# Kernel optimization log

Measured on AMD Instinct MI355X. Metric: run time of the kernel, lower is better.

## Reference

```python
import jax, jax.numpy as jnp
import numpy as np
from jax import lax

B, T, E, H, D, L = 2048, 512, 128, 8, 16, 3


def _ln(x, g, b):
    m = jnp.mean(x, -1, keepdims=True)
    v = jnp.var(x, -1, keepdims=True)
    return (x - m) / jnp.sqrt(v + 1e-5) * g + b


def _bn(x, g, b):  # eval-mode BatchNorm2d with running_mean=0, running_var=1
    return x * (g / np.sqrt(1.0 + 1e-5))[None, :, None, None] + b[None, :, None, None]


def _conv(x, w, b):  # 3x3 conv, padding=1, NCHW / OIHW
    y = lax.conv_general_dilated(x, w, (1, 1), 'SAME', dimension_numbers=('NCHW', 'OIHW', 'NCHW'))
    return y + b[None, :, None, None]


def _forward(enc_out, x1, x2, x3, c11_w, c11_b, bn11_g, bn11_b, c12_w, c12_b, bn12_g, bn12_b,
             fc1_w, fc1_b, c21_w, c21_b, bn21_g, bn21_b, fc2_w, fc2_b, fc_w, fc_b,
             wk, wq, wv, proj_w, proj_b, ln1_g, ln1_b, ln2_g, ln2_b, ln3_g, ln3_b, ln4_g, ln4_b,
             ff_w1, ff_b1, ff_w2, ff_b2, lnf_g, lnf_b, head_w, head_b):
    # StateNet -> query vector q: [B, E]
    h1 = jax.nn.relu(_bn(_conv(x1, c11_w, c11_b), bn11_g, bn11_b))
    h1 = jax.nn.relu(_bn(_conv(h1, c12_w, c12_b), bn12_g, bn12_b))
    h1 = jax.nn.relu(h1.reshape(h1.shape[0], -1) @ fc1_w + fc1_b)  # [B, 64]
    h2 = jax.nn.relu(_bn(_conv(x2, c21_w, c21_b), bn21_g, bn21_b))
    h2 = jax.nn.relu(h2.reshape(h2.shape[0], -1) @ fc2_w + fc2_b)  # [B, 16]
    q = jax.nn.relu(jnp.concatenate([h1, h2, x3], axis=-1) @ fc_w + fc_b)  # [B, E]

    for l in range(L):  # 3 structurally identical DecoderBlocks
        kx = _ln(enc_out, ln1_g[l], ln1_b[l])
        vx = _ln(enc_out, ln2_g[l], ln2_b[l])
        qx = _ln(q, ln3_g[l], ln3_b[l])
        K = (kx @ wk[l]).reshape(B, T, H, D)
        V = (vx @ wv[l]).reshape(B, T, H, D)
        Q = (qx @ wq[l]).reshape(B, H, D)
        # NOTE: original multiplies (not divides) by head_size**0.5 -- kept faithful.
        wei = jax.nn.softmax(jnp.einsum('bhd,bthd->bht', Q, K) * (D ** 0.5), axis=-1)
        att = jnp.einsum('bht,bthd->bhd', wei, V).reshape(B, E)
        q = q + att @ proj_w[l] + proj_b[l]
        h = _ln(q, ln4_g[l], ln4_b[l])
        q = q + jax.nn.gelu(h @ ff_w1[l] + ff_b1[l], approximate=False) @ ff_w2[l] + ff_b2[l]

    x = _ln(q, lnf_g, lnf_b)
    return x @ head_w + head_b  # discard head logits [B, 37]


def setup_inputs():
    key = jax.random.key(0)
    ks = iter(jax.random.split(key, 32))
    r = lambda *s: jax.random.normal(next(ks), s, jnp.float32) * 0.02
    z = lambda *s: jnp.zeros(s, jnp.float32)
    o = lambda *s: jnp.ones(s, jnp.float32)
    return dict(
        enc_out=jax.random.normal(next(ks), (B, T, E), jnp.float32),
        x1=jax.random.normal(next(ks), (B, 3, 37, 1), jnp.float32),
        x2=jax.random.normal(next(ks), (B, 7, 4, 1), jnp.float32),
        x3=jax.random.normal(next(ks), (B, 4), jnp.float32),
        c11_w=r(8, 3, 3, 3), c11_b=z(8), bn11_g=o(8), bn11_b=z(8),
        c12_w=r(8, 8, 3, 3), c12_b=z(8), bn12_g=o(8), bn12_b=z(8),
        fc1_w=r(296, 64), fc1_b=z(64),
        c21_w=r(8, 7, 3, 3), c21_b=z(8), bn21_g=o(8), bn21_b=z(8),
        fc2_w=r(32, 16), fc2_b=z(16),
        fc_w=r(84, E), fc_b=z(E),
        wk=r(L, E, E), wq=r(L, E, E), wv=r(L, E, E),
        proj_w=r(L, E, E), proj_b=z(L, E),
        ln1_g=o(L, E), ln1_b=z(L, E), ln2_g=o(L, E), ln2_b=z(L, E),
        ln3_g=o(L, E), ln3_b=z(L, E), ln4_g=o(L, E), ln4_b=z(L, E),
        ff_w1=r(L, E, 4 * E), ff_b1=z(L, 4 * E), ff_w2=r(L, 4 * E, E), ff_b2=z(L, E),
        lnf_g=o(E), lnf_b=z(E),
        head_w=r(E, 37), head_b=z(37),
    )


def reference(enc_out, x1, x2, x3, c11_w, c11_b, bn11_g, bn11_b, c12_w, c12_b, bn12_g, bn12_b,
              fc1_w, fc1_b, c21_w, c21_b, bn21_g, bn21_b, fc2_w, fc2_b, fc_w, fc_b,
              wk, wq, wv, proj_w, proj_b, ln1_g, ln1_b, ln2_g, ln2_b, ln3_g, ln3_b, ln4_g, ln4_b,
              ff_w1, ff_b1, ff_w2, ff_b2, lnf_g, lnf_b, head_w, head_b):
    return _forward(enc_out, x1, x2, x3, c11_w, c11_b, bn11_g, bn11_b, c12_w, c12_b, bn12_g, bn12_b,
                    fc1_w, fc1_b, c21_w, c21_b, bn21_g, bn21_b, fc2_w, fc2_b, fc_w, fc_b,
                    wk, wq, wv, proj_w, proj_b, ln1_g, ln1_b, ln2_g, ln2_b, ln3_g, ln3_b, ln4_g, ln4_b,
                    ff_w1, ff_b1, ff_w2, ff_b2, lnf_g, lnf_b, head_w, head_b)
```

## Files before the change

kernel.cpp:

```cpp
#include <hip/hip_runtime.h>
#include <math.h>

typedef unsigned int u32;
typedef unsigned short u16;
typedef unsigned char u8;
typedef __attribute__((ext_vector_type(4))) float f32x4;
typedef __attribute__((ext_vector_type(8))) short bf16x8;

__device__ __forceinline__ u16 f2b(float f){ u32 u=__float_as_uint(f); u=(u+0x7fffu+((u>>16)&1u))>>16; return (u16)u; }
__device__ __forceinline__ float b2f(u16 h){ return __uint_as_float(((u32)h)<<16); }

struct P {
  const float* in[43];
  float* out;
  float* q;
  u16*   S;
  const u16* xr;
  u16*   xw;
  int    xstrideu;
};

__global__ __launch_bounds__(512) void k_state(P p){
  __shared__ float sx1[112];
  __shared__ float sx2[32];
  __shared__ float sa[296];
  __shared__ float sb[296];
  __shared__ float sc2[32];
  __shared__ float sh1[64];
  __shared__ float sh2[16];
  __shared__ float red[512];
  int tid=threadIdx.x; int b=blockIdx.x;
  const float rs_bn = rsqrtf(1.0f+1e-5f);
  const float* x1 = p.in[1] + (size_t)b*111;
  const float* x2 = p.in[2] + (size_t)b*28;
  if (tid<111) sx1[tid]=x1[tid];
  if (tid>=128 && tid<156) sx2[tid-128]=x2[tid-128];
  __syncthreads();
  if (tid<296){
    int cc=tid/37, i=tid-cc*37;
    const float* wgt=p.in[4];
    float acc=p.in[5][cc];
    #pragma unroll
    for(int ic=0;ic<3;++ic)
      #pragma unroll
      for(int kh=0;kh<3;++kh){
        int ii=i+kh-1;
        if((unsigned)ii<37u) acc+=wgt[((cc*3+ic)*3+kh)*3+1]*sx1[ic*37+ii];
      }
    acc=acc*(p.in[6][cc]*rs_bn)+p.in[7][cc];
    sa[tid]=fmaxf(acc,0.f);
  }
  if (tid>=296 && tid<328){
    int o=tid-296, cc=o>>2, i=o&3;
    const float* wgt=p.in[14];
    float acc=p.in[15][cc];
    for(int ic=0;ic<7;++ic)
      for(int kh=0;kh<3;++kh){
        int ii=i+kh-1;
        if((unsigned)ii<4u) acc+=wgt[((cc*7+ic)*3+kh)*3+1]*sx2[ic*4+ii];
      }
    acc=acc*(p.in[16][cc]*rs_bn)+p.in[17][cc];
    sc2[o]=fmaxf(acc,0.f);
  }
  __syncthreads();
  if (tid<296){
    int cc=tid/37, i=tid-cc*37;
    const float* wgt=p.in[8];
    float acc=p.in[9][cc];
    #pragma unroll
    for(int ic=0;ic<8;++ic)
      #pragma unroll
      for(int kh=0;kh<3;++kh){
        int ii=i+kh-1;
        if((unsigned)ii<37u) acc+=wgt[((cc*8+ic)*3+kh)*3+1]*sa[ic*37+ii];
      }
    acc=acc*(p.in[10][cc]*rs_bn)+p.in[11][cc];
    sb[tid]=fmaxf(acc,0.f);
  }
  if (tid>=480 && tid<496){
    int o=tid-480;
    const float* wgt=p.in[18];
    float acc=p.in[19][o];
    for(int k=0;k<32;++k) acc+=sc2[k]*wgt[k*16+o];
    sh2[o]=fmaxf(acc,0.f);
  }
  __syncthreads();
  {
    int o=tid>>3, j=tid&7;
    const float* wgt=p.in[12];
    float part=0.f;
    for(int m=0;m<37;++m){ int k=j*37+m; part+=sb[k]*wgt[k*64+o]; }
    red[o*8+j]=part;
  }
  __syncthreads();
  if (tid<64){
    float acc=p.in[13][tid];
    #pragma unroll
    for(int j=0;j<8;++j) acc+=red[tid*8+j];
    sh1[tid]=fmaxf(acc,0.f);
  }
  __syncthreads();
  if (tid<128){
    const float* wgt=p.in[20];
    const float* x3=p.in[3]+(size_t)b*4;
    float acc=p.in[21][tid];
    for(int k=0;k<64;++k) acc+=sh1[k]*wgt[k*128+tid];
    for(int k=0;k<16;++k) acc+=sh2[k]*wgt[(64+k)*128+tid];
    #pragma unroll
    for(int k=0;k<4;++k) acc+=x3[k]*wgt[(80+k)*128+tid];
    p.q[(size_t)b*128+tid]=fmaxf(acc,0.f);
  }
}

__global__ __launch_bounds__(256) void k_xhat(P p){
  int b = blockIdx.x; int tid=threadIdx.x; int w=tid>>6, lane=tid&63;
  int r2 = lane>>5, c = lane&31;
  const float* enc = p.in[0] + (size_t)b*512*128;
  u16* xw = p.xw + (size_t)b*512*p.xstrideu;
  for (int it=0; it<64; ++it){
    int row = w*128 + it*2 + r2;
    float4 v = *(const float4*)(enc + (size_t)row*128 + c*4);
    float s = v.x+v.y+v.z+v.w;
    float s2 = v.x*v.x+v.y*v.y+v.z*v.z+v.w*v.w;
    #pragma unroll
    for (int m=1; m<=16; m<<=1){ s+=__shfl_xor(s,m); s2+=__shfl_xor(s2,m); }
    float mean = s*(1.f/128.f);
    float rstd = rsqrtf(s2*(1.f/128.f)-mean*mean+1e-5f);
    u32 a = (u32)f2b((v.x-mean)*rstd) | ((u32)f2b((v.y-mean)*rstd)<<16);
    u32 bq= (u32)f2b((v.z-mean)*rstd) | ((u32)f2b((v.w-mean)*rstd)<<16);
    *(uint2*)(xw + (size_t)row*p.xstrideu + c*4) = make_uint2(a,bq);
  }
}

#define XS 136
__global__ __launch_bounds__(256,3) void k_attn(P p, int l){
  __shared__ u16 XH[128*XS];
  __shared__ u16 WT[16*XS];
  __shared__ u16 QK[16*XS];
  __shared__ float qxs[128], Qs[128], red[256];
  __shared__ float wred[64], sred[64], alphaL[16], mL[16], m_run[16], invL[16], st[2];
  int tid=threadIdx.x, w=tid>>6, lane=tid&63, l15=lane&15, q4=lane>>4;
  int b = blockIdx.x;
  const float* wk = p.in[22] + l*16384;
  const float* wq = p.in[23] + l*16384;
  const float* g1 = p.in[27] + l*128;
  const float* g2 = p.in[29] + l*128;
  const float* g3 = p.in[31] + l*128;
  const float* b3 = p.in[32] + l*128;
  const float* qg = p.q + (size_t)b*128;

  if (w==0){
    float x0=qg[lane], x1=qg[lane+64];
    float s=x0+x1, s2=x0*x0+x1*x1;
    #pragma unroll
    for(int m=1;m<=32;m<<=1){ s+=__shfl_xor(s,m); s2+=__shfl_xor(s2,m); }
    if(lane==0){ float mean=s*(1.f/128.f); st[0]=mean; st[1]=rsqrtf(s2*(1.f/128.f)-mean*mean+1e-5f); }
  }
  if (tid<16) m_run[tid] = -INFINITY;
  __syncthreads();
  if (tid<128) qxs[tid] = (qg[tid]-st[0])*st[1]*g3[tid] + b3[tid];
  __syncthreads();
  {
    int o = tid & 127, kh = tid>>7;
    float acc=0;
    const float* wp = wq + kh*64*128 + o;
    #pragma unroll 8
    for (int e=0;e<64;++e) acc += qxs[kh*64+e]*wp[e*128];
    red[tid]=acc;
  }
  __syncthreads();
  if (tid<128) Qs[tid]=red[tid]+red[tid+128];
  for (int i=tid; i<8*XS; i+=256) QK[8*XS+i]=0;
  __syncthreads();
  {
    int h = tid>>5, e0=(tid&31)*4;
    float Qh[16];
    #pragma unroll
    for(int d=0;d<16;++d) Qh[d]=Qs[h*16+d];
    #pragma unroll
    for(int j=0;j<4;++j){
      int e=e0+j;
      const float* wr = wk + e*128 + h*16;
      float4 w0=*(const float4*)(wr), w1=*(const float4*)(wr+4), w2=*(const float4*)(wr+8), w3=*(const float4*)(wr+12);
      float acc = Qh[0]*w0.x+Qh[1]*w0.y+Qh[2]*w0.z+Qh[3]*w0.w
                + Qh[4]*w1.x+Qh[5]*w1.y+Qh[6]*w1.z+Qh[7]*w1.w
                + Qh[8]*w2.x+Qh[9]*w2.y+Qh[10]*w2.z+Qh[11]*w2.w
                + Qh[12]*w3.x+Qh[13]*w3.y+Qh[14]*w3.z+Qh[15]*w3.w;
      QK[h*XS+e] = f2b(acc*g1[e]*4.f);
    }
  }
  __syncthreads();
  bf16x8 qkf[4];
  #pragma unroll
  for(int ks=0;ks<4;++ks) qkf[ks]=*(const bf16x8*)(QK + l15*XS + ks*32 + q4*8);

  const u16* xrow = p.xr + (size_t)b*512*p.xstrideu;
  f32x4 wa0={0,0,0,0}, wa1={0,0,0,0};
  float s_part=0.f;
  for (int ch=0; ch<4; ++ch){
    __syncthreads();
    {
      const u16* src = xrow + (size_t)ch*128*p.xstrideu;
      #pragma unroll
      for(int i=0;i<8;++i){
        int idx = tid + i*256;
        int row = idx>>4, oct = idx&15;
        uint4 v = *(const uint4*)(src + (size_t)row*p.xstrideu + oct*8);
        *(uint4*)(XH + row*XS + oct*8) = v;
      }
    }
    __syncthreads();
    f32x4 c0={0,0,0,0}, c1={0,0,0,0};
    #pragma unroll
    for(int ks=0;ks<4;++ks){
      bf16x8 a0 = *(const bf16x8*)(XH + (w*32+l15)*XS + ks*32 + q4*8);
      bf16x8 a1 = *(const bf16x8*)(XH + (w*32+16+l15)*XS + ks*32 + q4*8);
      c0 = __builtin_amdgcn_mfma_f32_16x16x32_bf16(a0, qkf[ks], c0, 0,0,0);
      c1 = __builtin_amdgcn_mfma_f32_16x16x32_bf16(a1, qkf[ks], c1, 0,0,0);
    }
    float mx = fmaxf(fmaxf(fmaxf(c0[0],c0[1]),fmaxf(c0[2],c0[3])),
                     fmaxf(fmaxf(c1[0],c1[1]),fmaxf(c1[2],c1[3])));
    mx = fmaxf(mx, __shfl_xor(mx,16)); mx = fmaxf(mx, __shfl_xor(mx,32));
    if (lane<16) wred[w*16+lane]=mx;
    __syncthreads();
    if (tid<16){
      float m_new = fmaxf(fmaxf(wred[tid],wred[16+tid]),fmaxf(wred[32+tid],wred[48+tid]));
      m_new = fmaxf(m_new, m_run[tid]);
      alphaL[tid] = __expf(m_run[tid]-m_new);
      mL[tid]=m_new; m_run[tid]=m_new;
    }
    __syncthreads();
    float mnew = mL[l15];
    float e0v[4], e1v[4];
    float ssum=0.f;
    #pragma unroll
    for(int r=0;r<4;++r){ e0v[r]=__expf(c0[r]-mnew); e1v[r]=__expf(c1[r]-mnew); ssum+=e0v[r]+e1v[r]; }
    #pragma unroll
    for(int r=0;r<4;++r){
      WT[l15*XS + w*32 + q4*4 + r]      = f2b(e0v[r]);
      WT[l15*XS + w*32 + 16 + q4*4 + r] = f2b(e1v[r]);
    }
    ssum += __shfl_xor(ssum,16); ssum += __shfl_xor(ssum,32);
    s_part = s_part*alphaL[l15] + ssum;
    float ar0=alphaL[q4*4+0], ar1=alphaL[q4*4+1], ar2=alphaL[q4*4+2], ar3=alphaL[q4*4+3];
    wa0[0]*=ar0; wa0[1]*=ar1; wa0[2]*=ar2; wa0[3]*=ar3;
    wa1[0]*=ar0; wa1[1]*=ar1; wa1[2]*=ar2; wa1[3]*=ar3;
    __syncthreads();
    int eb0 = w*32 + l15, eb1 = w*32 + 16 + l15;
    #pragma unroll
    for(int ks=0;ks<4;++ks){
      bf16x8 aw = *(const bf16x8*)(WT + l15*XS + ks*32 + q4*8);
      bf16x8 bb0, bb1;
      #pragma unroll
      for(int j=0;j<8;++j){
        int t = ks*32 + q4*8 + j;
        bb0[j] = (short)XH[t*XS + eb0];
        bb1[j] = (short)XH[t*XS + eb1];
      }
      wa0 = __builtin_amdgcn_mfma_f32_16x16x32_bf16(aw, bb0, wa0, 0,0,0);
      wa1 = __builtin_amdgcn_mfma_f32_16x16x32_bf16(aw, bb1, wa1, 0,0,0);
    }
  }
  if (lane<16) sred[w*16+lane]=s_part;
  __syncthreads();
  if (tid<16) invL[tid] = 1.f/(sred[tid]+sred[16+tid]+sred[32+tid]+sred[48+tid]);
  __syncthreads();
  {
    int e0 = w*32 + l15, e1 = w*32+16+l15;
    float g20 = g2[e0], g21 = g2[e1];
    u16* Sb = p.S + (size_t)b*1024;
    #pragma unroll
    for(int r=0;r<4;++r){
      int h = q4*4+r;
      if (h<8){
        Sb[h*128 + e0] = f2b(wa0[r]*invL[h]*g20);
        Sb[h*128 + e1] = f2b(wa1[r]*invL[h]*g21);
      }
    }
  }
}

__global__ __launch_bounds__(256) void k_post(P p, int l){
  __shared__ u16 Ss[8*8*136];
  __shared__ float atts[8*128];
  __shared__ float qps[8*128];
  __shared__ float qx4[8*128];
  __shared__ float us[8*512];
  __shared__ float b2s[128];
  int tid=threadIdx.x; int r=tid>>5, c=tid&31;
  int b8 = blockIdx.x*8;
  const float* wv = p.in[24] + l*16384;
  const float* pw = p.in[25] + l*16384;
  const float* pb = p.in[26] + l*128;
  const float* b2 = p.in[30] + l*128;
  const float* g4 = p.in[33] + l*128;
  const float* b4 = p.in[34] + l*128;
  const float* f1 = p.in[35] + l*65536;
  const float* fb1= p.in[36] + l*512;
  const float* f2 = p.in[37] + l*65536;
  const float* fb2= p.in[38] + l*128;

  {
    const u16* Sg = p.S + (size_t)(b8+r)*1024;
    #pragma unroll
    for(int j=0;j<4;++j){
      int idx = c*8 + j*256;
      uint4 v = *(const uint4*)(Sg + idx);
      int h = idx>>7, e = idx&127;
      *(uint4*)(Ss + (r*8+h)*136 + e) = v;
    }
  }
  if (tid<128) b2s[tid]=b2[tid];
  __syncthreads();
  {
    int o0=c*4; int h=c>>2;
    float a0=0,a1=0,a2=0,a3=0, cc0=0,cc1=0,cc2=0,cc3=0;
    const u16* Sr = Ss + (r*8+h)*136;
    for(int e=0;e<128;++e){
      float sv=b2f(Sr[e]);
      float bv=b2s[e];
      float4 w4=*(const float4*)(wv + e*128 + o0);
      a0+=sv*w4.x; a1+=sv*w4.y; a2+=sv*w4.z; a3+=sv*w4.w;
      cc0+=bv*w4.x; cc1+=bv*w4.y; cc2+=bv*w4.z; cc3+=bv*w4.w;
    }
    atts[r*128+o0]=a0+cc0; atts[r*128+o0+1]=a1+cc1; atts[r*128+o0+2]=a2+cc2; atts[r*128+o0+3]=a3+cc3;
  }
  __syncthreads();
  {
    int o0=c*4;
    float a0=0,a1=0,a2=0,a3=0;
    for(int e=0;e<128;++e){
      float av=atts[r*128+e];
      float4 w4=*(const float4*)(pw + e*128 + o0);
      a0+=av*w4.x; a1+=av*w4.y; a2+=av*w4.z; a3+=av*w4.w;
    }
    float4 qv4=*(const float4*)(p.q + (size_t)(b8+r)*128 + o0);
    float4 pb4=*(const float4*)(pb + o0);
    qps[r*128+o0]  =qv4.x+a0+pb4.x;
    qps[r*128+o0+1]=qv4.y+a1+pb4.y;
    qps[r*128+o0+2]=qv4.z+a2+pb4.z;
    qps[r*128+o0+3]=qv4.w+a3+pb4.w;
  }
  __syncthreads();
  {
    float v0=qps[r*128+c], v1=qps[r*128+c+32], v2=qps[r*128+c+64], v3=qps[r*128+c+96];
    float s=v0+v1+v2+v3, s2=v0*v0+v1*v1+v2*v2+v3*v3;
    #pragma unroll
    for(int m=1;m<=16;m<<=1){ s+=__shfl_xor(s,m); s2+=__shfl_xor(s2,m); }
    float mean=s*(1.f/128.f), rstd=rsqrtf(s2*(1.f/128.f)-mean*mean+1e-5f);
    qx4[r*128+c]    =(v0-mean)*rstd*g4[c]+b4[c];
    qx4[r*128+c+32] =(v1-mean)*rstd*g4[c+32]+b4[c+32];
    qx4[r*128+c+64] =(v2-mean)*rstd*g4[c+64]+b4[c+64];
    qx4[r*128+c+96] =(v3-mean)*rstd*g4[c+96]+b4[c+96];
  }
  __syncthreads();
  {
    float acc[4][4]={};
    for(int e=0;e<128;++e){
      float xv=qx4[r*128+e];
      #pragma unroll
      for(int j=0;j<4;++j){
        float4 w4=*(const float4*)(f1 + e*512 + j*128 + c*4);
        acc[j][0]+=xv*w4.x; acc[j][1]+=xv*w4.y; acc[j][2]+=xv*w4.z; acc[j][3]+=xv*w4.w;
      }
    }
    #pragma unroll
    for(int j=0;j<4;++j)
      #pragma unroll
      for(int k=0;k<4;++k){
        int o=j*128+c*4+k;
        float u=acc[j][k]+fb1[o];
        us[r*512+o]=0.5f*u*(1.f+erff(u*0.70710678118654752f));
      }
  }
  __syncthreads();
  {
    int o0=c*4;
    float a0=0,a1=0,a2=0,a3=0;
    for(int e=0;e<512;++e){
      float uv=us[r*512+e];
      float4 w4=*(const float4*)(f2 + e*128 + o0);
      a0+=uv*w4.x; a1+=uv*w4.y; a2+=uv*w4.z; a3+=uv*w4.w;
    }
    float4 fb=*(const float4*)(fb2+o0);
    float* qp = p.q + (size_t)(b8+r)*128 + o0;
    float o0v=qps[r*128+o0]+a0+fb.x;
    float o1v=qps[r*128+o0+1]+a1+fb.y;
    float o2v=qps[r*128+o0+2]+a2+fb.z;
    float o3v=qps[r*128+o0+3]+a3+fb.w;
    float4 res; res.x=o0v; res.y=o1v; res.z=o2v; res.w=o3v;
    *(float4*)qp = res;
  }
}

__global__ __launch_bounds__(256) void k_head(P p){
  __shared__ float qx[8*128];
  int tid=threadIdx.x; int r=tid>>5, c=tid&31;
  int b8=blockIdx.x*8;
  const float* lg=p.in[39]; const float* lb=p.in[40];
  const float* hw=p.in[41]; const float* hb=p.in[42];
  const float* qp=p.q+(size_t)(b8+r)*128;
  float v0=qp[c],v1=qp[c+32],v2=qp[c+64],v3=qp[c+96];
  float s=v0+v1+v2+v3, s2=v0*v0+v1*v1+v2*v2+v3*v3;
  #pragma unroll
  for(int m=1;m<=16;m<<=1){ s+=__shfl_xor(s,m); s2+=__shfl_xor(s2,m); }
  float mean=s*(1.f/128.f), rstd=rsqrtf(s2*(1.f/128.f)-mean*mean+1e-5f);
  qx[r*128+c]   =(v0-mean)*rstd*lg[c]+lb[c];
  qx[r*128+c+32]=(v1-mean)*rstd*lg[c+32]+lb[c+32];
  qx[r*128+c+64]=(v2-mean)*rstd*lg[c+64]+lb[c+64];
  qx[r*128+c+96]=(v3-mean)*rstd*lg[c+96]+lb[c+96];
  __syncthreads();
  #pragma unroll
  for(int j=0;j<2;++j){
    int o=c+32*j;
    if(o<37){
      float acc=hb[o];
      #pragma unroll 4
      for(int e=0;e<128;++e) acc+=qx[r*128+e]*hw[e*37+o];
      p.out[(size_t)(b8+r)*37+o]=acc;
    }
  }
}

extern "C" void kernel_launch(void* const* d_in, const int* in_sizes, int n_in,
                              void* d_out, int out_size, void* d_ws, size_t ws_size,
                              hipStream_t stream) {
  (void)in_sizes; (void)n_in; (void)out_size;
  P pa;
  for(int i=0;i<43;++i) pa.in[i]=(const float*)d_in[i];
  pa.out=(float*)d_out;
  u8* ws=(u8*)d_ws;
  pa.q=(float*)ws;
  pa.S=(u16*)(ws + (1u<<20));
  size_t xbytes = (size_t)2048*512*256;
  if (ws_size >= (size_t)(8u<<20) + xbytes){
    pa.xw=(u16*)(ws+(8u<<20)); pa.xstrideu=128;
  } else {
    pa.xw=(u16*)d_in[0];       pa.xstrideu=256;
  }
  pa.xr = pa.xw;
  k_state<<<2048,512,0,stream>>>(pa);
  k_xhat<<<2048,256,0,stream>>>(pa);
  for(int l=0;l<3;++l){
    k_attn<<<2048,256,0,stream>>>(pa,l);
    k_post<<<256,256,0,stream>>>(pa,l);
  }
  k_head<<<256,256,0,stream>>>(pa);
}
```

Before: 1.308 ms.

## Fuse layernorm, all decoder layers and head into one persistent per-batch kernel

Replaces the separate xhat, per-layer attention, per-layer post-processing and head kernels with a single kernel per batch element. The normalized encoder tile (512x128 bf16) stays resident in LDS across all three layers, so the normalized activations are never written to and re-read from global memory three times. It also uses a single-pass softmax over all 512 tokens instead of the chunked online softmax. The cost is one 512-thread block per CU with about 157 KB of LDS, low occupancy, and the MLP GEMVs now run per batch row instead of amortised over 8 rows, so weights are re-read for every batch element.

After: 1.448 ms. 1.11x slower.

```diff
diff --git a/kernel.cpp b/kernel.cpp
--- a/kernel.cpp
+++ b/kernel.cpp
@@ -14,10 +14,6 @@
   const float* in[43];
   float* out;
   float* q;
-  u16*   S;
-  const u16* xr;
-  u16*   xw;
-  int    xstrideu;
 };
 
 __global__ __launch_bounds__(512) void k_state(P p){
@@ -112,338 +108,288 @@
   }
 }
 
-__global__ __launch_bounds__(256) void k_xhat(P p){
-  int b = blockIdx.x; int tid=threadIdx.x; int w=tid>>6, lane=tid&63;
-  int r2 = lane>>5, c = lane&31;
-  const float* enc = p.in[0] + (size_t)b*512*128;
-  u16* xw = p.xw + (size_t)b*512*p.xstrideu;
-  for (int it=0; it<64; ++it){
-    int row = w*128 + it*2 + r2;
-    float4 v = *(const float4*)(enc + (size_t)row*128 + c*4);
-    float s = v.x+v.y+v.z+v.w;
-    float s2 = v.x*v.x+v.y*v.y+v.z*v.z+v.w*v.w;
-    #pragma unroll
-    for (int m=1; m<=16; m<<=1){ s+=__shfl_xor(s,m); s2+=__shfl_xor(s2,m); }
-    float mean = s*(1.f/128.f);
-    float rstd = rsqrtf(s2*(1.f/128.f)-mean*mean+1e-5f);
-    u32 a = (u32)f2b((v.x-mean)*rstd) | ((u32)f2b((v.y-mean)*rstd)<<16);
-    u32 bq= (u32)f2b((v.z-mean)*rstd) | ((u32)f2b((v.w-mean)*rstd)<<16);
-    *(uint2*)(xw + (size_t)row*p.xstrideu + c*4) = make_uint2(a,bq);
-  }
-}
-
-#define XS 136
-__global__ __launch_bounds__(256,3) void k_attn(P p, int l){
-  __shared__ u16 XH[128*XS];
-  __shared__ u16 WT[16*XS];
-  __shared__ u16 QK[16*XS];
-  __shared__ float qxs[128], Qs[128], red[256];
-  __shared__ float wred[64], sred[64], alphaL[16], mL[16], m_run[16], invL[16], st[2];
-  int tid=threadIdx.x, w=tid>>6, lane=tid&63, l15=lane&15, q4=lane>>4;
+#define FUSED_LDS 157184
+
+__global__ __launch_bounds__(512,1) void k_fused(P p){
+  extern __shared__ u8 sm[];
+  u16*  XH   = (u16*)sm;
+  u8*   WTU  = sm + 139264;
+  float* qv   = (float*)(sm + 155904);
+  float* wred = (float*)(sm + 156416);
+  float* mrow = (float*)(sm + 156928);
+  float* invL = (float*)(sm + 156992);
+  float* st   = (float*)(sm + 157056);
+
+  float* red  = (float*)(WTU);
+  float* qxs  = (float*)(WTU + 2048);
+  float* Qs   = (float*)(WTU + 2560);
+  u16*  QKb   = (u16*)(WTU + 3072);
+  u16*  WT    = (u16*)(WTU);
+  float* SS   = (float*)(WTU);
+  float* red2 = (float*)(WTU + 4224);
+  float* atts = (float*)(WTU + 6272);
+  float* qps  = (float*)(WTU + 6784);
+  float* qx4  = (float*)(WTU + 7296);
+  float* us   = (float*)(WTU + 7808);
+
+  int tid=threadIdx.x;
+  int w = tid>>6, lane = tid&63, l15 = lane&15, q4 = lane>>4;
   int b = blockIdx.x;
-  const float* wk = p.in[22] + l*16384;
-  const float* wq = p.in[23] + l*16384;
-  const float* g1 = p.in[27] + l*128;
-  const float* g2 = p.in[29] + l*128;
-  const float* g3 = p.in[31] + l*128;
-  const float* b3 = p.in[32] + l*128;
-  const float* qg = p.q + (size_t)b*128;
+
+  {
+    const float* enc = p.in[0] + (size_t)b*512*128;
+    int g = tid>>5, c = tid&31;
+    #pragma unroll 4
+    for (int it=0; it<32; ++it){
+      int row = it*16 + g;
+      float4 v = *(const float4*)(enc + (size_t)row*128 + c*4);
+      float s = v.x+v.y+v.z+v.w;
+      float s2 = v.x*v.x+v.y*v.y+v.z*v.z+v.w*v.w;
+      #pragma unroll
+      for (int m=1; m<=16; m<<=1){ s+=__shfl_xor(s,m); s2+=__shfl_xor(s2,m); }
+      float mean = s*(1.f/128.f);
+      float rstd = rsqrtf(s2*(1.f/128.f)-mean*mean+1e-5f);
+      u32 a = (u32)f2b((v.x-mean)*rstd) | ((u32)f2b((v.y-mean)*rstd)<<16);
+      u32 bq= (u32)f2b((v.z-mean)*rstd) | ((u32)f2b((v.w-mean)*rstd)<<16);
+      *(uint2*)(XH + row*136 + c*4) = make_uint2(a,bq);
+    }
+    if (tid<128) qv[tid] = p.q[(size_t)b*128 + tid];
+  }
+  __syncthreads();
+
+  for (int l=0; l<3; ++l){
+    const float* wk = p.in[22] + l*16384;
+    const float* wq = p.in[23] + l*16384;
+    const float* wv = p.in[24] + l*16384;
+    const float* pw = p.in[25] + l*16384;
+    const float* pb = p.in[26] + l*128;
+    const float* g1 = p.in[27] + l*128;
+    const float* g2 = p.in[29] + l*128;
+    const float* b2v= p.in[30] + l*128;
+    const float* g3 = p.in[31] + l*128;
+    const float* b3 = p.in[32] + l*128;
+    const float* g4 = p.in[33] + l*128;
+    const float* b4 = p.in[34] + l*128;
+    const float* f1 = p.in[35] + l*65536;
+    const float* fb1= p.in[36] + l*512;
+    const float* f2 = p.in[37] + l*65536;
+    const float* fb2= p.in[38] + l*128;
+
+    if (w==0){
+      float x0=qv[lane], x1=qv[lane+64];
+      float s=x0+x1, s2=x0*x0+x1*x1;
+      #pragma unroll
+      for(int m=1;m<=32;m<<=1){ s+=__shfl_xor(s,m); s2+=__shfl_xor(s2,m); }
+      if(lane==0){ float mean=s*(1.f/128.f); st[0]=mean; st[1]=rsqrtf(s2*(1.f/128.f)-mean*mean+1e-5f); }
+    }
+    __syncthreads();
+    if (tid<128) qxs[tid]=(qv[tid]-st[0])*st[1]*g3[tid]+b3[tid];
+    __syncthreads();
+
+    {
+      int o = tid&127, kk = tid>>7;
+      float acc=0.f;
+      const float* wp = wq + kk*32*128 + o;
+      #pragma unroll 8
+      for (int e=0;e<32;++e) acc += qxs[kk*32+e]*wp[e*128];
+      red[tid]=acc;
+    }
+    __syncthreads();
+    if (tid<128) Qs[tid]=red[tid]+red[tid+128]+red[tid+256]+red[tid+384];
+    __syncthreads();
+
+    {
+      int h = tid>>5, e0=(tid&31)*4;
+      if (h<8){
+        float Qh[16];
+        #pragma unroll
+        for(int d=0;d<16;++d) Qh[d]=Qs[h*16+d];
+        #pragma unroll
+        for(int j=0;j<4;++j){
+          int e=e0+j;
+          const float* wr = wk + e*128 + h*16;
+          float4 wv0=*(const float4*)(wr), wv1=*(const float4*)(wr+4), wv2=*(const float4*)(wr+8), wv3=*(const float4*)(wr+12);
+          float acc = Qh[0]*wv0.x+Qh[1]*wv0.y+Qh[2]*wv0.z+Qh[3]*wv0.w
+                    + Qh[4]*wv1.x+Qh[5]*wv1.y+Qh[6]*wv1.z+Qh[7]*wv1.w
+                    + Qh[8]*wv2.x+Qh[9]*wv2.y+Qh[10]*wv2.z+Qh[11]*wv2.w
+                    + Qh[12]*wv3.x+Qh[13]*wv3.y+Qh[14]*wv3.z+Qh[15]*wv3.w;
+          QKb[h*136+e] = f2b(acc*g1[e]*4.f);
+        }
+      } else {
+        #pragma unroll
+        for(int j=0;j<4;++j) QKb[h*136+e0+j]=0;
+      }
+    }
+    __syncthreads();
+
+    bf16x8 qkf[4];
+    #pragma unroll
+    for(int ks=0;ks<4;++ks) qkf[ks]=*(const bf16x8*)(QKb + l15*136 + ks*32 + q4*8);
+
+    f32x4 sc[4];
+    #pragma unroll
+    for(int mb=0;mb<4;++mb){
+      f32x4 c = {0.f,0.f,0.f,0.f};
+      #pragma unroll
+      for(int ks=0;ks<4;++ks){
+        bf16x8 a = *(const bf16x8*)(XH + (64*w + 16*mb + l15)*136 + ks*32 + q4*8);
+        c = __builtin_amdgcn_mfma_f32_16x16x32_bf16(a, qkf[ks], c, 0,0,0);
+      }
+      sc[mb]=c;
+    }
+    {
+      float mx = -INFINITY;
+      #pragma unroll
+      for(int mb=0;mb<4;++mb)
+        #pragma unroll
+        for(int r=0;r<4;++r) mx = fmaxf(mx, sc[mb][r]);
+      mx = fmaxf(mx, __shfl_xor(mx,16)); mx = fmaxf(mx, __shfl_xor(mx,32));
+      if (lane<16) wred[w*16+lane]=mx;
+    }
+    __syncthreads();
+    if (tid<16){
+      float m0=wred[tid];
+      #pragma unroll
+      for(int ww=1;ww<8;++ww) m0=fmaxf(m0, wred[ww*16+tid]);
+      mrow[tid]=m0;
+    }
+    __syncthreads();
+    {
+      float mh = mrow[l15];
+      float ssum=0.f;
+      #pragma unroll
+      for(int mb=0;mb<4;++mb)
+        #pragma unroll
+        for(int r=0;r<4;++r){
+          int t = 64*w + 16*mb + q4*4 + r;
+          float pv = __expf(sc[mb][r]-mh);
+          ssum += pv;
+          WT[l15*520 + t] = f2b(pv);
+        }
+      ssum += __shfl_xor(ssum,16); ssum += __shfl_xor(ssum,32);
+      if (lane<16) wred[w*16+lane]=ssum;
+    }
+    __syncthreads();
+    if (tid<16) invL[tid] = 1.f/(wred[tid]+wred[16+tid]+wred[32+tid]+wred[48+tid]
+                                +wred[64+tid]+wred[80+tid]+wred[96+tid]+wred[112+tid]);
+    __syncthreads();
+
+    f32x4 wa = {0.f,0.f,0.f,0.f};
+    int eb = w*16 + l15;
+    #pragma unroll 4
+    for(int ks=0;ks<16;++ks){
+      bf16x8 aw = *(const bf16x8*)(WT + l15*520 + ks*32 + q4*8);
+      bf16x8 bb;
+      #pragma unroll
+      for(int j=0;j<8;++j){
+        int t = ks*32 + q4*8 + j;
+        bb[j] = (short)XH[t*136 + eb];
+      }
+      wa = __builtin_amdgcn_mfma_f32_16x16x32_bf16(aw, bb, wa, 0,0,0);
+    }
+    __syncthreads();
+    if (q4 < 2){
+      float g2e = g2[eb], b2e = b2v[eb];
+      #pragma unroll
+      for(int r=0;r<4;++r){
+        int h = q4*4+r;
+        SS[h*132+eb] = wa[r]*invL[h]*g2e + b2e;
+      }
+    }
+    __syncthreads();
+
+    {
+      int o = tid&127, kk = tid>>7; int h=o>>4;
+      float acc=0.f;
+      const float* wp = wv + kk*32*128 + o;
+      const float* Sr = SS + h*132 + kk*32;
+      #pragma unroll 8
+      for(int e=0;e<32;++e) acc += Sr[e]*wp[e*128];
+      red2[tid]=acc;
+    }
+    __syncthreads();
+    if (tid<128) atts[tid]=red2[tid]+red2[tid+128]+red2[tid+256]+red2[tid+384];
+    __syncthreads();
+
+    {
+      int o = tid&127, kk = tid>>7;
+      float acc=0.f;
+      const float* wp = pw + kk*32*128 + o;
+      #pragma unroll 8
+      for(int e=0;e<32;++e) acc += atts[kk*32+e]*wp[e*128];
+      red2[tid]=acc;
+    }
+    __syncthreads();
+    if (tid<128) qps[tid]= qv[tid] + pb[tid] + red2[tid]+red2[tid+128]+red2[tid+256]+red2[tid+384];
+    __syncthreads();
+
+    if (w==0){
+      float x0=qps[lane], x1=qps[lane+64];
+      float s=x0+x1, s2=x0*x0+x1*x1;
+      #pragma unroll
+      for(int m=1;m<=32;m<<=1){ s+=__shfl_xor(s,m); s2+=__shfl_xor(s2,m); }
+      if(lane==0){ float mean=s*(1.f/128.f); st[0]=mean; st[1]=rsqrtf(s2*(1.f/128.f)-mean*mean+1e-5f); }
+    }
+    __syncthreads();
+    if (tid<128) qx4[tid]=(qps[tid]-st[0])*st[1]*g4[tid]+b4[tid];
+    __syncthreads();
+
+    {
+      int o = tid;
+      float acc=fb1[o];
+      const float* wp = f1 + o;
+      #pragma unroll 8
+      for(int e=0;e<128;++e) acc += qx4[e]*wp[e*512];
+      us[o]=0.5f*acc*(1.f+erff(acc*0.70710678118654752f));
+    }
+    __syncthreads();
+
+    {
+      int o = tid&127, kk = tid>>7;
+      float acc=0.f;
+      const float* wp = f2 + kk*128*128 + o;
+      #pragma unroll 8
+      for(int e=0;e<128;++e) acc += us[kk*128+e]*wp[e*128];
+      red2[tid]=acc;
+    }
+    __syncthreads();
+    if (tid<128) qv[tid]= qps[tid] + fb2[tid] + red2[tid]+red2[tid+128]+red2[tid+256]+red2[tid+384];
+    __syncthreads();
+  }
 
   if (w==0){
-    float x0=qg[lane], x1=qg[lane+64];
+    float x0=qv[lane], x1=qv[lane+64];
     float s=x0+x1, s2=x0*x0+x1*x1;
     #pragma unroll
     for(int m=1;m<=32;m<<=1){ s+=__shfl_xor(s,m); s2+=__shfl_xor(s2,m); }
     if(lane==0){ float mean=s*(1.f/128.f); st[0]=mean; st[1]=rsqrtf(s2*(1.f/128.f)-mean*mean+1e-5f); }
   }
-  if (tid<16) m_run[tid] = -INFINITY;
-  __syncthreads();
-  if (tid<128) qxs[tid] = (qg[tid]-st[0])*st[1]*g3[tid] + b3[tid];
-  __syncthreads();
-  {
-    int o = tid & 127, kh = tid>>7;
-    float acc=0;
-    const float* wp = wq + kh*64*128 + o;
-    #pragma unroll 8
-    for (int e=0;e<64;++e) acc += qxs[kh*64+e]*wp[e*128];
-    red[tid]=acc;
-  }
-  __syncthreads();
-  if (tid<128) Qs[tid]=red[tid]+red[tid+128];
-  for (int i=tid; i<8*XS; i+=256) QK[8*XS+i]=0;
-  __syncthreads();
-  {
-    int h = tid>>5, e0=(tid&31)*4;
-    float Qh[16];
-    #pragma unroll
-    for(int d=0;d<16;++d) Qh[d]=Qs[h*16+d];
-    #pragma unroll
-    for(int j=0;j<4;++j){
-      int e=e0+j;
-      const float* wr = wk + e*128 + h*16;
-      float4 w0=*(const float4*)(wr), w1=*(const float4*)(wr+4), w2=*(const float4*)(wr+8), w3=*(const float4*)(wr+12);
-      float acc = Qh[0]*w0.x+Qh[1]*w0.y+Qh[2]*w0.z+Qh[3]*w0.w
-                + Qh[4]*w1.x+Qh[5]*w1.y+Qh[6]*w1.z+Qh[7]*w1.w
-                + Qh[8]*w2.x+Qh[9]*w2.y+Qh[10]*w2.z+Qh[11]*w2.w
-                + Qh[12]*w3.x+Qh[13]*w3.y+Qh[14]*w3.z+Qh[15]*w3.w;
-      QK[h*XS+e] = f2b(acc*g1[e]*4.f);
-    }
-  }
-  __syncthreads();
-  bf16x8 qkf[4];
-  #pragma unroll
-  for(int ks=0;ks<4;++ks) qkf[ks]=*(const bf16x8*)(QK + l15*XS + ks*32 + q4*8);
-
-  const u16* xrow = p.xr + (size_t)b*512*p.xstrideu;
-  f32x4 wa0={0,0,0,0}, wa1={0,0,0,0};
-  float s_part=0.f;
-  for (int ch=0; ch<4; ++ch){
-    __syncthreads();
-    {
-      const u16* src = xrow + (size_t)ch*128*p.xstrideu;
-      #pragma unroll
-      for(int i=0;i<8;++i){
-        int idx = tid + i*256;
-        int row = idx>>4, oct = idx&15;
-        uint4 v = *(const uint4*)(src + (size_t)row*p.xstrideu + oct*8);
-        *(uint4*)(XH + row*XS + oct*8) = v;
-      }
-    }
-    __syncthreads();
-    f32x4 c0={0,0,0,0}, c1={0,0,0,0};
-    #pragma unroll
-    for(int ks=0;ks<4;++ks){
-      bf16x8 a0 = *(const bf16x8*)(XH + (w*32+l15)*XS + ks*32 + q4*8);
-      bf16x8 a1 = *(const bf16x8*)(XH + (w*32+16+l15)*XS + ks*32 + q4*8);
-      c0 = __builtin_amdgcn_mfma_f32_16x16x32_bf16(a0, qkf[ks], c0, 0,0,0);
-      c1 = __builtin_amdgcn_mfma_f32_16x16x32_bf16(a1, qkf[ks], c1, 0,0,0);
-    }
-    float mx = fmaxf(fmaxf(fmaxf(c0[0],c0[1]),fmaxf(c0[2],c0[3])),
-                     fmaxf(fmaxf(c1[0],c1[1]),fmaxf(c1[2],c1[3])));
-    mx = fmaxf(mx, __shfl_xor(mx,16)); mx = fmaxf(mx, __shfl_xor(mx,32));
-    if (lane<16) wred[w*16+lane]=mx;
-    __syncthreads();
-    if (tid<16){
-      float m_new = fmaxf(fmaxf(wred[tid],wred[16+tid]),fmaxf(wred[32+tid],wred[48+tid]));
-      m_new = fmaxf(m_new, m_run[tid]);
-      alphaL[tid] = __expf(m_run[tid]-m_new);
-      mL[tid]=m_new; m_run[tid]=m_new;
-    }
-    __syncthreads();
-    float mnew = mL[l15];
-    float e0v[4], e1v[4];
-    float ssum=0.f;
-    #pragma unroll
-    for(int r=0;r<4;++r){ e0v[r]=__expf(c0[r]-mnew); e1v[r]=__expf(c1[r]-mnew); ssum+=e0v[r]+e1v[r]; }
-    #pragma unroll
-    for(int r=0;r<4;++r){
-      WT[l15*XS + w*32 + q4*4 + r]      = f2b(e0v[r]);
-      WT[l15*XS + w*32 + 16 + q4*4 + r] = f2b(e1v[r]);
-    }
-    ssum += __shfl_xor(ssum,16); ssum += __shfl_xor(ssum,32);
-    s_part = s_part*alphaL[l15] + ssum;
-    float ar0=alphaL[q4*4+0], ar1=alphaL[q4*4+1], ar2=alphaL[q4*4+2], ar3=alphaL[q4*4+3];
-    wa0[0]*=ar0; wa0[1]*=ar1; wa0[2]*=ar2; wa0[3]*=ar3;
-    wa1[0]*=ar0; wa1[1]*=ar1; wa1[2]*=ar2; wa1[3]*=ar3;
-    __syncthreads();
-    int eb0 = w*32 + l15, eb1 = w*32 + 16 + l15;
-    #pragma unroll
-    for(int ks=0;ks<4;++ks){
-      bf16x8 aw = *(const bf16x8*)(WT + l15*XS + ks*32 + q4*8);
-      bf16x8 bb0, bb1;
-      #pragma unroll
-      for(int j=0;j<8;++j){
-        int t = ks*32 + q4*8 + j;
-        bb0[j] = (short)XH[t*XS + eb0];
-        bb1[j] = (short)XH[t*XS + eb1];
-      }
-      wa0 = __builtin_amdgcn_mfma_f32_16x16x32_bf16(aw, bb0, wa0, 0,0,0);
-      wa1 = __builtin_amdgcn_mfma_f32_16x16x32_bf16(aw, bb1, wa1, 0,0,0);
-    }
-  }
-  if (lane<16) sred[w*16+lane]=s_part;
-  __syncthreads();
-  if (tid<16) invL[tid] = 1.f/(sred[tid]+sred[16+tid]+sred[32+tid]+sred[48+tid]);
-  __syncthreads();
-  {
-    int e0 = w*32 + l15, e1 = w*32+16+l15;
-    float g20 = g2[e0], g21 = g2[e1];
-    u16* Sb = p.S + (size_t)b*1024;
-    #pragma unroll
-    for(int r=0;r<4;++r){
-      int h = q4*4+r;
-      if (h<8){
-        Sb[h*128 + e0] = f2b(wa0[r]*invL[h]*g20);
-        Sb[h*128 + e1] = f2b(wa1[r]*invL[h]*g21);
-      }
-    }
-  }
-}
-
-__global__ __launch_bounds__(256) void k_post(P p, int l){
-  __shared__ u16 Ss[8*8*136];
-  __shared__ float atts[8*128];
-  __shared__ float qps[8*128];
-  __shared__ float qx4[8*128];
-  __shared__ float us[8*512];
-  __shared__ float b2s[128];
-  int tid=threadIdx.x; int r=tid>>5, c=tid&31;
-  int b8 = blockIdx.x*8;
-  const float* wv = p.in[24] + l*16384;
-  const float* pw = p.in[25] + l*16384;
-  const float* pb = p.in[26] + l*128;
-  const float* b2 = p.in[30] + l*128;
-  const float* g4 = p.in[33] + l*128;
-  const float* b4 = p.in[34] + l*128;
-  const float* f1 = p.in[35] + l*65536;
-  const float* fb1= p.in[36] + l*512;
-  const float* f2 = p.in[37] + l*65536;
-  const float* fb2= p.in[38] + l*128;
-
-  {
-    const u16* Sg = p.S + (size_t)(b8+r)*1024;
-    #pragma unroll
-    for(int j=0;j<4;++j){
-      int idx = c*8 + j*256;
-      uint4 v = *(const uint4*)(Sg + idx);
-      int h = idx>>7, e = idx&127;
-      *(uint4*)(Ss + (r*8+h)*136 + e) = v;
-    }
-  }
-  if (tid<128) b2s[tid]=b2[tid];
-  __syncthreads();
-  {
-    int o0=c*4; int h=c>>2;
-    float a0=0,a1=0,a2=0,a3=0, cc0=0,cc1=0,cc2=0,cc3=0;
-    const u16* Sr = Ss + (r*8+h)*136;
-    for(int e=0;e<128;++e){
-      float sv=b2f(Sr[e]);
-      float bv=b2s[e];
-      float4 w4=*(const float4*)(wv + e*128 + o0);
-      a0+=sv*w4.x; a1+=sv*w4.y; a2+=sv*w4.z; a3+=sv*w4.w;
-      cc0+=bv*w4.x; cc1+=bv*w4.y; cc2+=bv*w4.z; cc3+=bv*w4.w;
-    }
-    atts[r*128+o0]=a0+cc0; atts[r*128+o0+1]=a1+cc1; atts[r*128+o0+2]=a2+cc2; atts[r*128+o0+3]=a3+cc3;
-  }
-  __syncthreads();
-  {
-    int o0=c*4;
-    float a0=0,a1=0,a2=0,a3=0;
-    for(int e=0;e<128;++e){
-      float av=atts[r*128+e];
-      float4 w4=*(const float4*)(pw + e*128 + o0);
-      a0+=av*w4.x; a1+=av*w4.y; a2+=av*w4.z; a3+=av*w4.w;
-    }
-    float4 qv4=*(const float4*)(p.q + (size_t)(b8+r)*128 + o0);
-    float4 pb4=*(const float4*)(pb + o0);
-    qps[r*128+o0]  =qv4.x+a0+pb4.x;
-    qps[r*128+o0+1]=qv4.y+a1+pb4.y;
-    qps[r*128+o0+2]=qv4.z+a2+pb4.z;
-    qps[r*128+o0+3]=qv4.w+a3+pb4.w;
-  }
-  __syncthreads();
-  {
-    float v0=qps[r*128+c], v1=qps[r*128+c+32], v2=qps[r*128+c+64], v3=qps[r*128+c+96];
-    float s=v0+v1+v2+v3, s2=v0*v0+v1*v1+v2*v2+v3*v3;
-    #pragma unroll
-    for(int m=1;m<=16;m<<=1){ s+=__shfl_xor(s,m); s2+=__shfl_xor(s2,m); }
-    float mean=s*(1.f/128.f), rstd=rsqrtf(s2*(1.f/128.f)-mean*mean+1e-5f);
-    qx4[r*128+c]    =(v0-mean)*rstd*g4[c]+b4[c];
-    qx4[r*128+c+32] =(v1-mean)*rstd*g4[c+32]+b4[c+32];
-    qx4[r*128+c+64] =(v2-mean)*rstd*g4[c+64]+b4[c+64];
-    qx4[r*128+c+96] =(v3-mean)*rstd*g4[c+96]+b4[c+96];
-  }
-  __syncthreads();
-  {
-    float acc[4][4]={};
-    for(int e=0;e<128;++e){
-      float xv=qx4[r*128+e];
-      #pragma unroll
-      for(int j=0;j<4;++j){
-        float4 w4=*(const float4*)(f1 + e*512 + j*128 + c*4);
-        acc[j][0]+=xv*w4.x; acc[j][1]+=xv*w4.y; acc[j][2]+=xv*w4.z; acc[j][3]+=xv*w4.w;
-      }
-    }
-    #pragma unroll
-    for(int j=0;j<4;++j)
-      #pragma unroll
-      for(int k=0;k<4;++k){
-        int o=j*128+c*4+k;
-        float u=acc[j][k]+fb1[o];
-        us[r*512+o]=0.5f*u*(1.f+erff(u*0.70710678118654752f));
-      }
-  }
-  __syncthreads();
-  {
-    int o0=c*4;
-    float a0=0,a1=0,a2=0,a3=0;
-    for(int e=0;e<512;++e){
-      float uv=us[r*512+e];
-      float4 w4=*(const float4*)(f2 + e*128 + o0);
-      a0+=uv*w4.x; a1+=uv*w4.y; a2+=uv*w4.z; a3+=uv*w4.w;
-    }
-    float4 fb=*(const float4*)(fb2+o0);
-    float* qp = p.q + (size_t)(b8+r)*128 + o0;
-    float o0v=qps[r*128+o0]+a0+fb.x;
-    float o1v=qps[r*128+o0+1]+a1+fb.y;
-    float o2v=qps[r*128+o0+2]+a2+fb.z;
-    float o3v=qps[r*128+o0+3]+a3+fb.w;
-    float4 res; res.x=o0v; res.y=o1v; res.z=o2v; res.w=o3v;
-    *(float4*)qp = res;
-  }
-}
-
-__global__ __launch_bounds__(256) void k_head(P p){
-  __shared__ float qx[8*128];
-  int tid=threadIdx.x; int r=tid>>5, c=tid&31;
-  int b8=blockIdx.x*8;
-  const float* lg=p.in[39]; const float* lb=p.in[40];
-  const float* hw=p.in[41]; const float* hb=p.in[42];
-  const float* qp=p.q+(size_t)(b8+r)*128;
-  float v0=qp[c],v1=qp[c+32],v2=qp[c+64],v3=qp[c+96];
-  float s=v0+v1+v2+v3, s2=v0*v0+v1*v1+v2*v2+v3*v3;
-  #pragma unroll
-  for(int m=1;m<=16;m<<=1){ s+=__shfl_xor(s,m); s2+=__shfl_xor(s2,m); }
-  float mean=s*(1.f/128.f), rstd=rsqrtf(s2*(1.f/128.f)-mean*mean+1e-5f);
-  qx[r*128+c]   =(v0-mean)*rstd*lg[c]+lb[c];
-  qx[r*128+c+32]=(v1-mean)*rstd*lg[c+32]+lb[c+32];
-  qx[r*128+c+64]=(v2-mean)*rstd*lg[c+64]+lb[c+64];
-  qx[r*128+c+96]=(v3-mean)*rstd*lg[c+96]+lb[c+96];
-  __syncthreads();
-  #pragma unroll
-  for(int j=0;j<2;++j){
-    int o=c+32*j;
-    if(o<37){
-      float acc=hb[o];
-      #pragma unroll 4
-      for(int e=0;e<128;++e) acc+=qx[r*128+e]*hw[e*37+o];
-      p.out[(size_t)(b8+r)*37+o]=acc;
-    }
+  __syncthreads();
+  if (tid<128) qx4[tid]=(qv[tid]-st[0])*st[1]*p.in[39][tid]+p.in[40][tid];
+  __syncthreads();
+  if (tid<37){
+    const float* hw=p.in[41];
+    float acc=p.in[42][tid];
+    #pragma unroll 4
+    for(int e=0;e<128;++e) acc += qx4[e]*hw[e*37+tid];
+    p.out[(size_t)b*37+tid]=acc;
   }
 }
 
 extern "C" void kernel_launch(void* const* d_in, const int* in_sizes, int n_in,
                               void* d_out, int out_size, void* d_ws, size_t ws_size,
                               hipStream_t stream) {
-  (void)in_sizes; (void)n_in; (void)out_size;
+  (void)in_sizes; (void)n_in; (void)out_size; (void)ws_size;
   P pa;
   for(int i=0;i<43;++i) pa.in[i]=(const float*)d_in[i];
   pa.out=(float*)d_out;
-  u8* ws=(u8*)d_ws;
-  pa.q=(float*)ws;
-  pa.S=(u16*)(ws + (1u<<20));
-  size_t xbytes = (size_t)2048*512*256;
-  if (ws_size >= (size_t)(8u<<20) + xbytes){
-    pa.xw=(u16*)(ws+(8u<<20)); pa.xstrideu=128;
-  } else {
-    pa.xw=(u16*)d_in[0];       pa.xstrideu=256;
-  }
-  pa.xr = pa.xw;
+  pa.q=(float*)d_ws;
+  static bool inited=false;
+  if (!inited){
+    hipFuncSetAttribute(reinterpret_cast<const void*>(k_fused),
+                        hipFuncAttributeMaxDynamicSharedMemorySize, FUSED_LDS);
+    inited=true;
+  }
   k_state<<<2048,512,0,stream>>>(pa);
-  k_xhat<<<2048,256,0,stream>>>(pa);
-  for(int l=0;l<3;++l){
-    k_attn<<<2048,256,0,stream>>>(pa,l);
-    k_post<<<256,256,0,stream>>>(pa,l);
-  }
-  k_head<<<256,256,0,stream>>>(pa);
+  k_fused<<<2048,512,FUSED_LDS,stream>>>(pa);
 }
```

## Prefetch x chunks via registers, swizzle LDS, and use 512-thread attention blocks

Applied to the files above, without the earlier changes.

The attention kernel now runs 512 threads per block, so each wave handles 16 rows instead of 32. The next 128-row chunk of normalized encoder output is prefetched into registers while the current chunk is computed, overlapping global loads with MFMA work. An XOR swizzle is applied to LDS columns to reduce bank conflicts, and the softmax denominator is reduced in shared memory each chunk. The larger block and the extra staging registers may lower occupancy, and each chunk needs more barriers.

Measured after the change: 1.303 ms. Within noise of the previous version (-0.3%).

```diff
diff --git a/kernel.cpp b/kernel.cpp
--- a/kernel.cpp
+++ b/kernel.cpp
@@ -133,12 +133,13 @@
 }
 
 #define XS 136
-__global__ __launch_bounds__(256,3) void k_attn(P p, int l){
-  __shared__ u16 XH[128*XS];
+#define SWZ16(r) ((((r)>>3)&3)<<4)
+__global__ __launch_bounds__(512) void k_attn(P p, int l){
+  __shared__ u16 XB[128*XS];
   __shared__ u16 WT[16*XS];
   __shared__ u16 QK[16*XS];
-  __shared__ float qxs[128], Qs[128], red[256];
-  __shared__ float wred[64], sred[64], alphaL[16], mL[16], m_run[16], invL[16], st[2];
+  __shared__ float qxs[128], Qs[128], red[512], wred[128];
+  __shared__ float alphaL[16], mL[16], m_run[16], s_run[16], invL[16], st[2];
   int tid=threadIdx.x, w=tid>>6, lane=tid&63, l15=lane&15, q4=lane>>4;
   int b = blockIdx.x;
   const float* wk = p.in[22] + l*16384;
@@ -148,6 +149,17 @@
   const float* g3 = p.in[31] + l*128;
   const float* b3 = p.in[32] + l*128;
   const float* qg = p.q + (size_t)b*128;
+  const u16* xrow = p.xr + (size_t)b*512*p.xstrideu;
+
+  int srow = tid>>4, sg = tid&15;
+  uint4 stg0, stg1, stg2, stg3;
+  {
+    const u16* src = xrow;
+    stg0 = *(const uint4*)(src + (size_t)(srow   )*p.xstrideu + sg*8);
+    stg1 = *(const uint4*)(src + (size_t)(srow+32)*p.xstrideu + sg*8);
+    stg2 = *(const uint4*)(src + (size_t)(srow+64)*p.xstrideu + sg*8);
+    stg3 = *(const uint4*)(src + (size_t)(srow+96)*p.xstrideu + sg*8);
+  }
 
   if (w==0){
     float x0=qg[lane], x1=qg[lane+64];
@@ -156,30 +168,29 @@
     for(int m=1;m<=32;m<<=1){ s+=__shfl_xor(s,m); s2+=__shfl_xor(s2,m); }
     if(lane==0){ float mean=s*(1.f/128.f); st[0]=mean; st[1]=rsqrtf(s2*(1.f/128.f)-mean*mean+1e-5f); }
   }
-  if (tid<16) m_run[tid] = -INFINITY;
-  __syncthreads();
-  if (tid<128) qxs[tid] = (qg[tid]-st[0])*st[1]*g3[tid] + b3[tid];
-  __syncthreads();
-  {
-    int o = tid & 127, kh = tid>>7;
-    float acc=0;
-    const float* wp = wq + kh*64*128 + o;
+  if (tid<16){ m_run[tid]=-INFINITY; s_run[tid]=0.f; }
+  __syncthreads();
+  if (tid<128) qxs[tid]=(qg[tid]-st[0])*st[1]*g3[tid]+b3[tid];
+  __syncthreads();
+  {
+    int o = tid&127, kk = tid>>7;
+    float acc=0.f;
+    const float* wp = wq + kk*32*128 + o;
     #pragma unroll 8
-    for (int e=0;e<64;++e) acc += qxs[kh*64+e]*wp[e*128];
+    for (int e=0;e<32;++e) acc += qxs[kk*32+e]*wp[e*128];
     red[tid]=acc;
   }
   __syncthreads();
-  if (tid<128) Qs[tid]=red[tid]+red[tid+128];
-  for (int i=tid; i<8*XS; i+=256) QK[8*XS+i]=0;
-  __syncthreads();
-  {
-    int h = tid>>5, e0=(tid&31)*4;
+  if (tid<128) Qs[tid]=red[tid]+red[tid+128]+red[tid+256]+red[tid+384];
+  __syncthreads();
+  {
+    int h = tid>>6, i = tid&63;
     float Qh[16];
     #pragma unroll
     for(int d=0;d<16;++d) Qh[d]=Qs[h*16+d];
     #pragma unroll
-    for(int j=0;j<4;++j){
-      int e=e0+j;
+    for(int j=0;j<2;++j){
+      int e=i*2+j;
       const float* wr = wk + e*128 + h*16;
       float4 w0=*(const float4*)(wr), w1=*(const float4*)(wr+4), w2=*(const float4*)(wr+8), w3=*(const float4*)(wr+12);
       float acc = Qh[0]*w0.x+Qh[1]*w0.y+Qh[2]*w0.z+Qh[3]*w0.w
@@ -189,93 +200,99 @@
       QK[h*XS+e] = f2b(acc*g1[e]*4.f);
     }
   }
+  if (tid<256){ int h2=8+(tid>>5), e0=(tid&31)*4;
+    #pragma unroll
+    for(int j=0;j<4;++j) QK[h2*XS+e0+j]=0;
+  }
   __syncthreads();
   bf16x8 qkf[4];
   #pragma unroll
   for(int ks=0;ks<4;++ks) qkf[ks]=*(const bf16x8*)(QK + l15*XS + ks*32 + q4*8);
 
-  const u16* xrow = p.xr + (size_t)b*512*p.xstrideu;
-  f32x4 wa0={0,0,0,0}, wa1={0,0,0,0};
-  float s_part=0.f;
-  for (int ch=0; ch<4; ++ch){
+  f32x4 wa = {0.f,0.f,0.f,0.f};
+  int eb = w*16 + l15;
+  int ebs = eb ^ (q4<<4);
+  int swc = (sg*8) ^ SWZ16(srow);
+
+  for (int c=0; c<4; ++c){
+    *(uint4*)(XB + (srow   )*XS + swc) = stg0;
+    *(uint4*)(XB + (srow+32)*XS + swc) = stg1;
+    *(uint4*)(XB + (srow+64)*XS + swc) = stg2;
+    *(uint4*)(XB + (srow+96)*XS + swc) = stg3;
+    __syncthreads();
+    if (c<3){
+      const u16* src = xrow + (size_t)(c+1)*128*p.xstrideu;
+      stg0 = *(const uint4*)(src + (size_t)(srow   )*p.xstrideu + sg*8);
+      stg1 = *(const uint4*)(src + (size_t)(srow+32)*p.xstrideu + sg*8);
+      stg2 = *(const uint4*)(src + (size_t)(srow+64)*p.xstrideu + sg*8);
+      stg3 = *(const uint4*)(src + (size_t)(srow+96)*p.xstrideu + sg*8);
+    }
+    f32x4 sc = {0.f,0.f,0.f,0.f};
+    {
+      int r = 16*w + l15, s0 = SWZ16(r);
+      #pragma unroll
+      for(int ks=0;ks<4;++ks){
+        bf16x8 a = *(const bf16x8*)(XB + r*XS + ((ks*32 + q4*8)^s0));
+        sc = __builtin_amdgcn_mfma_f32_16x16x32_bf16(a, qkf[ks], sc, 0,0,0);
+      }
+    }
+    {
+      float mx = fmaxf(fmaxf(sc[0],sc[1]),fmaxf(sc[2],sc[3]));
+      mx = fmaxf(mx, __shfl_xor(mx,16)); mx = fmaxf(mx, __shfl_xor(mx,32));
+      if (lane<16) wred[w*16+lane]=mx;
+    }
+    __syncthreads();
+    if (tid<16){
+      float m0=m_run[tid];
+      #pragma unroll
+      for(int ww=0;ww<8;++ww) m0=fmaxf(m0, wred[ww*16+tid]);
+      alphaL[tid]=__expf(m_run[tid]-m0); mL[tid]=m0; m_run[tid]=m0;
+    }
     __syncthreads();
     {
-      const u16* src = xrow + (size_t)ch*128*p.xstrideu;
-      #pragma unroll
-      for(int i=0;i<8;++i){
-        int idx = tid + i*256;
-        int row = idx>>4, oct = idx&15;
-        uint4 v = *(const uint4*)(src + (size_t)row*p.xstrideu + oct*8);
-        *(uint4*)(XH + row*XS + oct*8) = v;
-      }
-    }
-    __syncthreads();
-    f32x4 c0={0,0,0,0}, c1={0,0,0,0};
-    #pragma unroll
-    for(int ks=0;ks<4;++ks){
-      bf16x8 a0 = *(const bf16x8*)(XH + (w*32+l15)*XS + ks*32 + q4*8);
-      bf16x8 a1 = *(const bf16x8*)(XH + (w*32+16+l15)*XS + ks*32 + q4*8);
-      c0 = __builtin_amdgcn_mfma_f32_16x16x32_bf16(a0, qkf[ks], c0, 0,0,0);
-      c1 = __builtin_amdgcn_mfma_f32_16x16x32_bf16(a1, qkf[ks], c1, 0,0,0);
-    }
-    float mx = fmaxf(fmaxf(fmaxf(c0[0],c0[1]),fmaxf(c0[2],c0[3])),
-                     fmaxf(fmaxf(c1[0],c1[1]),fmaxf(c1[2],c1[3])));
-    mx = fmaxf(mx, __shfl_xor(mx,16)); mx = fmaxf(mx, __shfl_xor(mx,32));
-    if (lane<16) wred[w*16+lane]=mx;
+      float mh = mL[l15];
+      float ssum=0.f;
+      float ev[4];
+      #pragma unroll
+      for(int r=0;r<4;++r){ ev[r]=__expf(sc[r]-mh); ssum+=ev[r]; }
+      #pragma unroll
+      for(int r=0;r<4;++r) WT[l15*XS + 16*w + q4*4 + r] = f2b(ev[r]);
+      ssum += __shfl_xor(ssum,16); ssum += __shfl_xor(ssum,32);
+      if (lane<16) wred[w*16+lane]=ssum;
+    }
+    {
+      float a0=alphaL[q4*4+0], a1=alphaL[q4*4+1], a2=alphaL[q4*4+2], a3=alphaL[q4*4+3];
+      wa[0]*=a0; wa[1]*=a1; wa[2]*=a2; wa[3]*=a3;
+    }
     __syncthreads();
     if (tid<16){
-      float m_new = fmaxf(fmaxf(wred[tid],wred[16+tid]),fmaxf(wred[32+tid],wred[48+tid]));
-      m_new = fmaxf(m_new, m_run[tid]);
-      alphaL[tid] = __expf(m_run[tid]-m_new);
-      mL[tid]=m_new; m_run[tid]=m_new;
-    }
-    __syncthreads();
-    float mnew = mL[l15];
-    float e0v[4], e1v[4];
-    float ssum=0.f;
-    #pragma unroll
-    for(int r=0;r<4;++r){ e0v[r]=__expf(c0[r]-mnew); e1v[r]=__expf(c1[r]-mnew); ssum+=e0v[r]+e1v[r]; }
-    #pragma unroll
-    for(int r=0;r<4;++r){
-      WT[l15*XS + w*32 + q4*4 + r]      = f2b(e0v[r]);
-      WT[l15*XS + w*32 + 16 + q4*4 + r] = f2b(e1v[r]);
-    }
-    ssum += __shfl_xor(ssum,16); ssum += __shfl_xor(ssum,32);
-    s_part = s_part*alphaL[l15] + ssum;
-    float ar0=alphaL[q4*4+0], ar1=alphaL[q4*4+1], ar2=alphaL[q4*4+2], ar3=alphaL[q4*4+3];
-    wa0[0]*=ar0; wa0[1]*=ar1; wa0[2]*=ar2; wa0[3]*=ar3;
-    wa1[0]*=ar0; wa1[1]*=ar1; wa1[2]*=ar2; wa1[3]*=ar3;
-    __syncthreads();
-    int eb0 = w*32 + l15, eb1 = w*32 + 16 + l15;
+      float s0=s_run[tid]*alphaL[tid];
+      #pragma unroll
+      for(int ww=0;ww<8;++ww) s0+=wred[ww*16+tid];
+      s_run[tid]=s0;
+    }
     #pragma unroll
     for(int ks=0;ks<4;++ks){
       bf16x8 aw = *(const bf16x8*)(WT + l15*XS + ks*32 + q4*8);
-      bf16x8 bb0, bb1;
+      bf16x8 bb;
       #pragma unroll
       for(int j=0;j<8;++j){
         int t = ks*32 + q4*8 + j;
-        bb0[j] = (short)XH[t*XS + eb0];
-        bb1[j] = (short)XH[t*XS + eb1];
-      }
-      wa0 = __builtin_amdgcn_mfma_f32_16x16x32_bf16(aw, bb0, wa0, 0,0,0);
-      wa1 = __builtin_amdgcn_mfma_f32_16x16x32_bf16(aw, bb1, wa1, 0,0,0);
-    }
-  }
-  if (lane<16) sred[w*16+lane]=s_part;
-  __syncthreads();
-  if (tid<16) invL[tid] = 1.f/(sred[tid]+sred[16+tid]+sred[32+tid]+sred[48+tid]);
-  __syncthreads();
-  {
-    int e0 = w*32 + l15, e1 = w*32+16+l15;
-    float g20 = g2[e0], g21 = g2[e1];
+        bb[j] = (short)XB[t*XS + ebs];
+      }
+      wa = __builtin_amdgcn_mfma_f32_16x16x32_bf16(aw, bb, wa, 0,0,0);
+    }
+    __syncthreads();
+  }
+  if (tid<16) invL[tid] = 1.f/s_run[tid];
+  __syncthreads();
+  if (q4<2){
+    float g2e = g2[eb];
     u16* Sb = p.S + (size_t)b*1024;
     #pragma unroll
     for(int r=0;r<4;++r){
       int h = q4*4+r;
-      if (h<8){
-        Sb[h*128 + e0] = f2b(wa0[r]*invL[h]*g20);
-        Sb[h*128 + e1] = f2b(wa1[r]*invL[h]*g21);
-      }
+      Sb[h*128 + eb] = f2b(wa[r]*invL[h]*g2e);
     }
   }
 }
@@ -442,7 +459,7 @@
   k_state<<<2048,512,0,stream>>>(pa);
   k_xhat<<<2048,256,0,stream>>>(pa);
   for(int l=0;l<3;++l){
-    k_attn<<<2048,256,0,stream>>>(pa,l);
+    k_attn<<<2048,512,0,stream>>>(pa,l);
     k_post<<<256,256,0,stream>>>(pa,l);
   }
   k_head<<<256,256,0,stream>>>(pa);
```
